# Kernel tuning notes

Measured on AMD Instinct MI355X. Metric: run time of the kernel, lower is better.

Reference implementation:

```python
import jax, jax.numpy as jnp
import numpy as np
from jax.scipy.special import logsumexp

VOCAB = 32000
NUM_STATE = 512
BATCH = 64
MAXLEN = 256


def setup_inputs() -> dict:
    key = jax.random.key(0)
    k1, k2, k3, k4 = jax.random.split(key, 4)
    sentences = jax.random.randint(k1, (BATCH, MAXLEN), 0, VOCAB, dtype=jnp.int64 if jax.config.jax_enable_x64 else jnp.int32)
    masks = jnp.ones((BATCH, MAXLEN), dtype=jnp.float32)
    # parameters: uniform(-0.5, 0.5) as in reset_parameter
    input_w = jax.random.uniform(k2, (VOCAB, NUM_STATE), jnp.float32, -0.5, 0.5)
    transition = jax.random.uniform(k3, (NUM_STATE, NUM_STATE), jnp.float32, -0.5, 0.5)
    begin = jax.random.uniform(k4, (NUM_STATE,), jnp.float32, -0.5, 0.5)
    return {"sentences": sentences, "masks": masks, "input_w": input_w,
            "transition": transition, "begin": begin}


def reference(sentences, masks, input_w, transition, begin):
    batch, maxlen = sentences.shape
    S = begin.shape[0]
    # emission log-probs: log_softmax over dim 0 (vocab axis) — as in original
    norm_input = jax.nn.log_softmax(input_w, axis=0)            # [V, S]
    emis = norm_input[sentences.T]                               # [maxlen, batch, S]
    T = jax.nn.log_softmax(transition, axis=-1)                  # [S, S]

    def bmv(bv):
        # logsumexp(T[None] + bv[:, None, :], axis=-1) -> [batch, S]
        return logsumexp(T[None, :, :] + bv[:, None, :], axis=-1)

    fwd0 = jnp.broadcast_to(jax.nn.log_softmax(begin, axis=0), (batch, S))
    m0 = bmv(fwd0)                                               # [batch, S]
    # NOTE: original normalizes over dim=0 (the BATCH axis) via logsoftmax0
    m1 = bmv(jax.nn.log_softmax(m0 + emis[0], axis=0))

    # Original loop bug replicated: pre_forward = mid_forwards[i-1], so the
    # recurrence is lagged: m_{i+1} = f(m_{i-1}, e_i) for i >= 1.
    def step(carry, e):
        a, b = carry                                             # a = m_{i-1}, b = m_i
        m = bmv(jax.nn.log_softmax(a + e, axis=0))               # m_{i+1}
        return (b, m), m

    (_, _), ms = jax.lax.scan(step, (m0, m1), emis[1:maxlen - 1])
    hidden = jnp.concatenate([m0[None], m1[None], ms], axis=0)   # [maxlen, batch, S]

    pred_prob = hidden + emis
    ppl = logsumexp(pred_prob, axis=-1) * masks.T                # [maxlen, batch]
    return jnp.sum(ppl)
```

## Files before the change

kernel.cpp:

```cpp
#include <hip/hip_runtime.h>
#include <math.h>

#define VV 32000
#define SS 512
#define BB 64
#define TT 256
#define NS 128
#define NPART 500
#define NCB 128
#define WSLOT (BB * SS)


__global__ void k_zero(float* __restrict__ out, float* __restrict__ colsum,
                       unsigned* __restrict__ flags) {
  const int t = threadIdx.x;
  if (t == 0) out[0] = 0.f;
  if (t < 256) flags[t] = 0u;
  colsum[t] = 0.f;
}

__global__ void k_colpart(const float* __restrict__ iw, float* __restrict__ psum) {
  const int blk = blockIdx.x;
  const int tid = threadIdx.x;
  const int cg = tid & 127;
  const int rh = tid >> 7;
  const int r0 = blk * 128 + rh * 64;
  const float4* iw4 = (const float4*)iw;
  float4 s = make_float4(0.f, 0.f, 0.f, 0.f);
  #pragma unroll 4
  for (int r = 0; r < 64; ++r) {
    float4 x = iw4[(size_t)(r0 + r) * 128 + cg];
    s.x += __expf(x.x); s.y += __expf(x.y); s.z += __expf(x.z); s.w += __expf(x.w);
  }
  ((float4*)psum)[(size_t)(blk * 2 + rh) * 128 + cg] = s;
}

__global__ void k_colreduce(const float* __restrict__ psum, float* __restrict__ colsum) {
  const int c = threadIdx.x;
  const int p0 = blockIdx.x * 20;
  float s = 0.f;
  #pragma unroll 5
  for (int p = 0; p < 20; ++p) s += psum[(size_t)(p0 + p) * SS + c];
  atomicAdd(&colsum[c], s);
}

__global__ void k_lse(const float* __restrict__ colsum, float* __restrict__ colLSE) {
  colLSE[threadIdx.x] = __logf(colsum[threadIdx.x]);
}

__global__ void k_begin(const float* __restrict__ begin, float* __restrict__ sb) {
  __shared__ float red[8];
  const int tid = threadIdx.x;
  float x = begin[tid];
  float m = x;
  #pragma unroll
  for (int o = 32; o; o >>= 1) m = fmaxf(m, __shfl_xor(m, o));
  if ((tid & 63) == 0) red[tid >> 6] = m;
  __syncthreads();
  float bm = red[0];
  for (int i = 1; i < 8; ++i) bm = fmaxf(bm, red[i]);
  __syncthreads();
  float e = __expf(x - bm);
  float s = e;
  #pragma unroll
  for (int o = 32; o; o >>= 1) s += __shfl_xor(s, o);
  if ((tid & 63) == 0) red[tid >> 6] = s;
  __syncthreads();
  float tot = 0.f;
  for (int i = 0; i < 8; ++i) tot += red[i];
  sb[tid] = e / tot;
}

__global__ void k_transP(const float* __restrict__ trans, const float* __restrict__ sb,
                         float* __restrict__ P, float* __restrict__ q0vec) {
  const int i = blockIdx.x;
  const int lane = threadIdx.x;
  const float* rp = trans + (size_t)i * SS;
  float xs[8];
  float m = -1e30f;
  #pragma unroll
  for (int cc = 0; cc < 8; ++cc) { xs[cc] = rp[cc * 64 + lane]; m = fmaxf(m, xs[cc]); }
  #pragma unroll
  for (int o = 32; o; o >>= 1) m = fmaxf(m, __shfl_xor(m, o));
  float s = 0.f;
  #pragma unroll
  for (int cc = 0; cc < 8; ++cc) s += __expf(xs[cc] - m);
  #pragma unroll
  for (int o = 32; o; o >>= 1) s += __shfl_xor(s, o);
  const float lse = m + __logf(s);
  float qa = 0.f;
  #pragma unroll
  for (int cc = 0; cc < 8; ++cc) {
    float p = __expf(xs[cc] - lse);
    P[(size_t)i * SS + cc * 64 + lane] = p;
    qa += p * sb[cc * 64 + lane];
  }
  #pragma unroll
  for (int o = 32; o; o >>= 1) qa += __shfl_xor(qa, o);
  if (lane == 0) q0vec[i] = qa;
}

__global__ __launch_bounds__(256) void k_persist(
    const float* __restrict__ P, const float* __restrict__ q0vec,
    const float* __restrict__ iw, const float* __restrict__ colLSE,
    const int* __restrict__ sent, float* __restrict__ wring,
    float* __restrict__ dotpart, unsigned* __restrict__ flags) {
  const int c = blockIdx.x & 1;
  const int g = blockIdx.x >> 1;
  const int lane = threadIdx.x & 63;
  const int h = __builtin_amdgcn_readfirstlane(threadIdx.x >> 6);
  const int i0 = g << 2;
  const int kmax = c ? 127 : 128;
  unsigned* const myflags = flags + (c << 7);

  const float4 cl = *(const float4*)(colLSE + i0);
  const float4* const P0 = (const float4*)(P + (size_t)(i0 + 0) * SS) + h * 32;
  const float4* const P1 = (const float4*)(P + (size_t)(i0 + 1) * SS) + h * 32;
  const float4* const P2 = (const float4*)(P + (size_t)(i0 + 2) * SS) + h * 32;
  const float4* const P3 = (const float4*)(P + (size_t)(i0 + 3) * SS) + h * 32;

  __shared__ float4 red[4][64];

  for (int k = 0; k <= kmax; ++k) {
    const int t0 = 2 * k;
    const int tw = t0 + c;
    const int td = tw - 1;
    const bool doW = (h == 0) && (tw <= 254);
    const bool doD = (h == 1) && (td >= 0);

    float4 ivW = make_float4(0.f, 0.f, 0.f, 0.f);
    float4 ivD = make_float4(0.f, 0.f, 0.f, 0.f);
    if (doW) {
      const int row = sent[lane * TT + tw];
      ivW = *(const float4*)(iw + (size_t)row * SS + i0);
    }
    if (doD) {
      const int row = sent[lane * TT + td];
      ivD = *(const float4*)(iw + (size_t)row * SS + i0);
    }

    if (k > 0) {
      __syncthreads();
      if (h == 0) {
        const unsigned tgt = (unsigned)k;
        for (;;) {
          const unsigned va = __hip_atomic_load(myflags + lane, __ATOMIC_RELAXED,
                                                __HIP_MEMORY_SCOPE_AGENT);
          const unsigned vb = __hip_atomic_load(myflags + 64 + lane, __ATOMIC_RELAXED,
                                                __HIP_MEMORY_SCOPE_AGENT);
          if (__all((va >= tgt) && (vb >= tgt))) break;
          __builtin_amdgcn_s_sleep(2);
        }
      }
      __syncthreads();
    }

    float a0 = 0.f, a1 = 0.f, a2 = 0.f, a3 = 0.f;
    if (t0 == 0) {
      if (h == 0) {
        a0 = q0vec[i0 + 0]; a1 = q0vec[i0 + 1];
        a2 = q0vec[i0 + 2]; a3 = q0vec[i0 + 3];
      }
    } else {
      const float4* wv = (const float4*)(wring + (size_t)(tw - 2) * WSLOT)
                         + (size_t)h * 32 * 64;
      float4 wr[32];
      #pragma unroll
      for (int u = 0; u < 32; ++u) wr[u] = wv[u * 64 + lane];
      #pragma unroll
      for (int u = 0; u < 32; ++u) {
        const float4 p0 = P0[u];
        const float4 p1 = P1[u];
        const float4 p2 = P2[u];
        const float4 p3 = P3[u];
        a0 += wr[u].x * p0.x + wr[u].y * p0.y + wr[u].z * p0.z + wr[u].w * p0.w;
        a1 += wr[u].x * p1.x + wr[u].y * p1.y + wr[u].z * p1.z + wr[u].w * p1.w;
        a2 += wr[u].x * p2.x + wr[u].y * p2.y + wr[u].z * p2.z + wr[u].w * p2.w;
        a3 += wr[u].x * p3.x + wr[u].y * p3.y + wr[u].z * p3.z + wr[u].w * p3.w;
      }
    }

    red[h][lane] = make_float4(a0, a1, a2, a3);
    __syncthreads();

    if (h < 2) {
      const float4 r0 = red[0][lane], r1 = red[1][lane];
      const float4 r2 = red[2][lane], r3 = red[3][lane];
      const float s0 = (r0.x + r1.x) + (r2.x + r3.x);
      const float s1 = (r0.y + r1.y) + (r2.y + r3.y);
      const float s2 = (r0.z + r1.z) + (r2.z + r3.z);
      const float s3 = (r0.w + r1.w) + (r2.w + r3.w);

      if (doW) {
        float w0 = s0 * __expf(ivW.x - cl.x);
        float w1 = s1 * __expf(ivW.y - cl.y);
        float w2 = s2 * __expf(ivW.z - cl.z);
        float w3 = s3 * __expf(ivW.w - cl.w);
        float c0 = w0, c1 = w1, c2 = w2, c3 = w3;
        #pragma unroll
        for (int o = 32; o; o >>= 1) {
          c0 += __shfl_xor(c0, o);
          c1 += __shfl_xor(c1, o);
          c2 += __shfl_xor(c2, o);
          c3 += __shfl_xor(c3, o);
        }
        union { float2 f; unsigned long long u; } lo, hi;
        lo.f = make_float2(w0 / c0, w1 / c1);
        hi.f = make_float2(w2 / c2, w3 / c3);
        unsigned long long* wd = (unsigned long long*)
            ((float4*)(wring + (size_t)tw * WSLOT) + (g * 64 + lane));
        __hip_atomic_store(wd, lo.u, __ATOMIC_RELAXED, __HIP_MEMORY_SCOPE_AGENT);
        __hip_atomic_store(wd + 1, hi.u, __ATOMIC_RELAXED, __HIP_MEMORY_SCOPE_AGENT);
        asm volatile("s_waitcnt vmcnt(0)" ::: "memory");
        if (lane == 0)
          __hip_atomic_store(&myflags[g], (unsigned)(k + 1), __ATOMIC_RELAXED,
                             __HIP_MEMORY_SCOPE_AGENT);
      }

      if (doD) {
        const float dp = s0 * __expf(ivD.x - cl.x)
                       + s1 * __expf(ivD.y - cl.y)
                       + s2 * __expf(ivD.z - cl.z)
                       + s3 * __expf(ivD.w - cl.w);
        dotpart[((size_t)td * NS + g) * BB + lane] = dp;
      }
    }
  }
}

__global__ void k_final(const float* __restrict__ dotpart, const float* __restrict__ masks,
                        float* __restrict__ out) {
  const int t = blockIdx.x;
  const int tid = threadIdx.x;
  const int b = tid & 63, g = tid >> 6;
  float sum = 0.f;
  for (int s = g; s < NS; s += 4) sum += dotpart[((size_t)t * NS + s) * BB + b];
  __shared__ float red[4][64];
  red[g][b] = sum;
  __syncthreads();
  if (g == 0) {
    float tot = (red[0][b] + red[1][b]) + (red[2][b] + red[3][b]);
    float v = __logf(tot) * masks[b * TT + t];
    #pragma unroll
    for (int o = 32; o; o >>= 1) v += __shfl_xor(v, o);
    if (b == 0) atomicAdd(out, v);
  }
}

extern "C" void kernel_launch(void* const* d_in, const int* in_sizes, int n_in,
                              void* d_out, int out_size, void* d_ws, size_t ws_size,
                              hipStream_t stream) {
  const int* sent = (const int*)d_in[0];
  const float* masks = (const float*)d_in[1];
  const float* iw = (const float*)d_in[2];
  const float* trans = (const float*)d_in[3];
  const float* begin = (const float*)d_in[4];
  float* out = (float*)d_out;
  float* ws = (float*)d_ws;

  float* P = ws;
  float* colLSE = P + 262144;
  float* psum = colLSE + 512;
  float* colsum = psum + 256000;
  float* sb = colsum + 512;
  float* q0vec = sb + 512;
  float* dotpart = q0vec + 512;
  unsigned* flags = (unsigned*)(dotpart + 2097152);
  float* wring = (float*)flags + 512;

  k_zero<<<1, 512, 0, stream>>>(out, colsum, flags);
  k_colpart<<<250, 256, 0, stream>>>(iw, psum);
  k_colreduce<<<25, 512, 0, stream>>>(psum, colsum);
  k_lse<<<1, 512, 0, stream>>>(colsum, colLSE);
  k_begin<<<1, 512, 0, stream>>>(begin, sb);
  k_transP<<<512, 64, 0, stream>>>(trans, sb, P, q0vec);

  {
    const float* Pp = P;
    const float* q0p = q0vec;
    const float* iwp = iw;
    const float* clp = colLSE;
    const int* sentp = sent;
    float* wrp = wring;
    float* dpp = dotpart;
    unsigned* fp = flags;
    void* args[] = {&Pp, &q0p, &iwp, &clp, &sentp, &wrp, &dpp, &fp};
    (void)hipLaunchCooperativeKernel((const void*)k_persist, dim3(256), dim3(256),
                                     args, 0, stream);
  }

  k_final<<<TT, 256, 0, stream>>>(dotpart, masks, out);
}
```

Baseline: 786.9 us.

## Fold small prep kernels and split per-step flag sync across waves

Removes the zero, log-sum-exp and begin-softmax kernels by folding their work into k_colpart, k_transP and the persistent kernel, which cuts launch overhead. Inside the persistent recurrence, each wave now polls the flags itself instead of relying on two block barriers around a single polling wave. The normalized-weight write is split across two waves with separate low and high flag arrays, and the reduction buffer is double-buffered so one barrier per step is enough. This shortens the per-step critical path of the serial chain, at the cost of more spin traffic on the flags from every wave.

```diff
diff --git a/kernel.cpp b/kernel.cpp
--- a/kernel.cpp
+++ b/kernel.cpp
@@ -6,22 +6,19 @@
 #define BB 64
 #define TT 256
 #define NS 128
-#define NPART 500
-#define NCB 128
 #define WSLOT (BB * SS)
 
 
-__global__ void k_zero(float* __restrict__ out, float* __restrict__ colsum,
-                       unsigned* __restrict__ flags) {
-  const int t = threadIdx.x;
-  if (t == 0) out[0] = 0.f;
-  if (t < 256) flags[t] = 0u;
-  colsum[t] = 0.f;
-}
-
-__global__ void k_colpart(const float* __restrict__ iw, float* __restrict__ psum) {
+__global__ void k_colpart(const float* __restrict__ iw, float* __restrict__ psum,
+                          float* __restrict__ out, float* __restrict__ colsum,
+                          unsigned* __restrict__ flags) {
   const int blk = blockIdx.x;
   const int tid = threadIdx.x;
+  if (blk == 0) {
+    if (tid == 0) out[0] = 0.f;
+    flags[tid] = 0u; flags[tid + 256] = 0u;
+    colsum[tid] = 0.f; colsum[tid + 256] = 0.f;
+  }
   const int cg = tid & 127;
   const int rh = tid >> 7;
   const int r0 = blk * 128 + rh * 64;
@@ -44,37 +41,23 @@
   atomicAdd(&colsum[c], s);
 }
 
-__global__ void k_lse(const float* __restrict__ colsum, float* __restrict__ colLSE) {
-  colLSE[threadIdx.x] = __logf(colsum[threadIdx.x]);
-}
-
-__global__ void k_begin(const float* __restrict__ begin, float* __restrict__ sb) {
-  __shared__ float red[8];
-  const int tid = threadIdx.x;
-  float x = begin[tid];
-  float m = x;
-  #pragma unroll
-  for (int o = 32; o; o >>= 1) m = fmaxf(m, __shfl_xor(m, o));
-  if ((tid & 63) == 0) red[tid >> 6] = m;
-  __syncthreads();
-  float bm = red[0];
-  for (int i = 1; i < 8; ++i) bm = fmaxf(bm, red[i]);
-  __syncthreads();
-  float e = __expf(x - bm);
-  float s = e;
-  #pragma unroll
-  for (int o = 32; o; o >>= 1) s += __shfl_xor(s, o);
-  if ((tid & 63) == 0) red[tid >> 6] = s;
-  __syncthreads();
-  float tot = 0.f;
-  for (int i = 0; i < 8; ++i) tot += red[i];
-  sb[tid] = e / tot;
-}
-
-__global__ void k_transP(const float* __restrict__ trans, const float* __restrict__ sb,
+__global__ void k_transP(const float* __restrict__ trans, const float* __restrict__ begin,
                          float* __restrict__ P, float* __restrict__ q0vec) {
   const int i = blockIdx.x;
   const int lane = threadIdx.x;
+  float bx[8];
+  float bm = -1e30f;
+  #pragma unroll
+  for (int cc = 0; cc < 8; ++cc) { bx[cc] = begin[cc * 64 + lane]; bm = fmaxf(bm, bx[cc]); }
+  #pragma unroll
+  for (int o = 32; o; o >>= 1) bm = fmaxf(bm, __shfl_xor(bm, o));
+  float bs = 0.f;
+  #pragma unroll
+  for (int cc = 0; cc < 8; ++cc) { bx[cc] = __expf(bx[cc] - bm); bs += bx[cc]; }
+  #pragma unroll
+  for (int o = 32; o; o >>= 1) bs += __shfl_xor(bs, o);
+  const float binv = 1.f / bs;
+
   const float* rp = trans + (size_t)i * SS;
   float xs[8];
   float m = -1e30f;
@@ -93,7 +76,7 @@
   for (int cc = 0; cc < 8; ++cc) {
     float p = __expf(xs[cc] - lse);
     P[(size_t)i * SS + cc * 64 + lane] = p;
-    qa += p * sb[cc * 64 + lane];
+    qa += p * (bx[cc] * binv);
   }
   #pragma unroll
   for (int o = 32; o; o >>= 1) qa += __shfl_xor(qa, o);
@@ -102,7 +85,7 @@
 
 __global__ __launch_bounds__(256) void k_persist(
     const float* __restrict__ P, const float* __restrict__ q0vec,
-    const float* __restrict__ iw, const float* __restrict__ colLSE,
+    const float* __restrict__ iw, const float* __restrict__ colsum,
     const int* __restrict__ sent, float* __restrict__ wring,
     float* __restrict__ dotpart, unsigned* __restrict__ flags) {
   const int c = blockIdx.x & 1;
@@ -111,22 +94,28 @@
   const int h = __builtin_amdgcn_readfirstlane(threadIdx.x >> 6);
   const int i0 = g << 2;
   const int kmax = c ? 127 : 128;
-  unsigned* const myflags = flags + (c << 7);
-
-  const float4 cl = *(const float4*)(colLSE + i0);
+  unsigned* const flagL = flags + (c << 7);
+  unsigned* const flagH = flags + 256 + (c << 7);
+  const int gp = (h << 5) + (lane & 31);
+
+  float4 cl;
+  cl.x = __logf(colsum[i0 + 0]); cl.y = __logf(colsum[i0 + 1]);
+  cl.z = __logf(colsum[i0 + 2]); cl.w = __logf(colsum[i0 + 3]);
+
   const float4* const P0 = (const float4*)(P + (size_t)(i0 + 0) * SS) + h * 32;
   const float4* const P1 = (const float4*)(P + (size_t)(i0 + 1) * SS) + h * 32;
   const float4* const P2 = (const float4*)(P + (size_t)(i0 + 2) * SS) + h * 32;
   const float4* const P3 = (const float4*)(P + (size_t)(i0 + 3) * SS) + h * 32;
 
-  __shared__ float4 red[4][64];
+  __shared__ float4 red[2][4][64];
 
   for (int k = 0; k <= kmax; ++k) {
+    const int rb = k & 1;
     const int t0 = 2 * k;
     const int tw = t0 + c;
     const int td = tw - 1;
-    const bool doW = (h == 0) && (tw <= 254);
-    const bool doD = (h == 1) && (td >= 0);
+    const bool doW = (h <= 1) && (tw <= 254);
+    const bool doD = (h == 2) && (td >= 0);
 
     float4 ivW = make_float4(0.f, 0.f, 0.f, 0.f);
     float4 ivD = make_float4(0.f, 0.f, 0.f, 0.f);
@@ -140,19 +129,15 @@
     }
 
     if (k > 0) {
-      __syncthreads();
-      if (h == 0) {
-        const unsigned tgt = (unsigned)k;
-        for (;;) {
-          const unsigned va = __hip_atomic_load(myflags + lane, __ATOMIC_RELAXED,
-                                                __HIP_MEMORY_SCOPE_AGENT);
-          const unsigned vb = __hip_atomic_load(myflags + 64 + lane, __ATOMIC_RELAXED,
-                                                __HIP_MEMORY_SCOPE_AGENT);
-          if (__all((va >= tgt) && (vb >= tgt))) break;
-          __builtin_amdgcn_s_sleep(2);
-        }
-      }
-      __syncthreads();
+      const unsigned tgt = (unsigned)k;
+      for (;;) {
+        const unsigned va = __hip_atomic_load(flagL + gp, __ATOMIC_RELAXED,
+                                              __HIP_MEMORY_SCOPE_AGENT);
+        const unsigned vb = __hip_atomic_load(flagH + gp, __ATOMIC_RELAXED,
+                                              __HIP_MEMORY_SCOPE_AGENT);
+        if (__all((va >= tgt) && (vb >= tgt))) break;
+      }
+      asm volatile("" ::: "memory");
     }
 
     float a0 = 0.f, a1 = 0.f, a2 = 0.f, a3 = 0.f;
@@ -180,50 +165,57 @@
       }
     }
 
-    red[h][lane] = make_float4(a0, a1, a2, a3);
+    red[rb][h][lane] = make_float4(a0, a1, a2, a3);
     __syncthreads();
 
-    if (h < 2) {
-      const float4 r0 = red[0][lane], r1 = red[1][lane];
-      const float4 r2 = red[2][lane], r3 = red[3][lane];
+    if (doW) {
+      const float4 r0 = red[rb][0][lane], r1 = red[rb][1][lane];
+      const float4 r2 = red[rb][2][lane], r3 = red[rb][3][lane];
+      unsigned long long* wd = (unsigned long long*)
+          ((float4*)(wring + (size_t)tw * WSLOT) + (g * 64 + lane));
+      if (h == 0) {
+        const float s0 = (r0.x + r1.x) + (r2.x + r3.x);
+        const float s1 = (r0.y + r1.y) + (r2.y + r3.y);
+        float w0 = s0 * __expf(ivW.x - cl.x);
+        float w1 = s1 * __expf(ivW.y - cl.y);
+        float c0 = w0, c1 = w1;
+        #pragma unroll
+        for (int o = 32; o; o >>= 1) { c0 += __shfl_xor(c0, o); c1 += __shfl_xor(c1, o); }
+        union { float2 f; unsigned long long u; } lo;
+        lo.f = make_float2(w0 / c0, w1 / c1);
+        __hip_atomic_store(wd, lo.u, __ATOMIC_RELAXED, __HIP_MEMORY_SCOPE_AGENT);
+        asm volatile("s_waitcnt vmcnt(0)" ::: "memory");
+        if (lane == 0)
+          __hip_atomic_store(&flagL[g], (unsigned)(k + 1), __ATOMIC_RELAXED,
+                             __HIP_MEMORY_SCOPE_AGENT);
+      } else {
+        const float s2 = (r0.z + r1.z) + (r2.z + r3.z);
+        const float s3 = (r0.w + r1.w) + (r2.w + r3.w);
+        float w2 = s2 * __expf(ivW.z - cl.z);
+        float w3 = s3 * __expf(ivW.w - cl.w);
+        float c2 = w2, c3 = w3;
+        #pragma unroll
+        for (int o = 32; o; o >>= 1) { c2 += __shfl_xor(c2, o); c3 += __shfl_xor(c3, o); }
+        union { float2 f; unsigned long long u; } hi;
+        hi.f = make_float2(w2 / c2, w3 / c3);
+        __hip_atomic_store(wd + 1, hi.u, __ATOMIC_RELAXED, __HIP_MEMORY_SCOPE_AGENT);
+        asm volatile("s_waitcnt vmcnt(0)" ::: "memory");
+        if (lane == 0)
+          __hip_atomic_store(&flagH[g], (unsigned)(k + 1), __ATOMIC_RELAXED,
+                             __HIP_MEMORY_SCOPE_AGENT);
+      }
+    } else if (doD) {
+      const float4 r0 = red[rb][0][lane], r1 = red[rb][1][lane];
+      const float4 r2 = red[rb][2][lane], r3 = red[rb][3][lane];
       const float s0 = (r0.x + r1.x) + (r2.x + r3.x);
       const float s1 = (r0.y + r1.y) + (r2.y + r3.y);
       const float s2 = (r0.z + r1.z) + (r2.z + r3.z);
       const float s3 = (r0.w + r1.w) + (r2.w + r3.w);
-
-      if (doW) {
-        float w0 = s0 * __expf(ivW.x - cl.x);
-        float w1 = s1 * __expf(ivW.y - cl.y);
-        float w2 = s2 * __expf(ivW.z - cl.z);
-        float w3 = s3 * __expf(ivW.w - cl.w);
-        float c0 = w0, c1 = w1, c2 = w2, c3 = w3;
-        #pragma unroll
-        for (int o = 32; o; o >>= 1) {
-          c0 += __shfl_xor(c0, o);
-          c1 += __shfl_xor(c1, o);
-          c2 += __shfl_xor(c2, o);
-          c3 += __shfl_xor(c3, o);
-        }
-        union { float2 f; unsigned long long u; } lo, hi;
-        lo.f = make_float2(w0 / c0, w1 / c1);
-        hi.f = make_float2(w2 / c2, w3 / c3);
-        unsigned long long* wd = (unsigned long long*)
-            ((float4*)(wring + (size_t)tw * WSLOT) + (g * 64 + lane));
-        __hip_atomic_store(wd, lo.u, __ATOMIC_RELAXED, __HIP_MEMORY_SCOPE_AGENT);
-        __hip_atomic_store(wd + 1, hi.u, __ATOMIC_RELAXED, __HIP_MEMORY_SCOPE_AGENT);
-        asm volatile("s_waitcnt vmcnt(0)" ::: "memory");
-        if (lane == 0)
-          __hip_atomic_store(&myflags[g], (unsigned)(k + 1), __ATOMIC_RELAXED,
-                             __HIP_MEMORY_SCOPE_AGENT);
-      }
-
-      if (doD) {
-        const float dp = s0 * __expf(ivD.x - cl.x)
-                       + s1 * __expf(ivD.y - cl.y)
-                       + s2 * __expf(ivD.z - cl.z)
-                       + s3 * __expf(ivD.w - cl.w);
-        dotpart[((size_t)td * NS + g) * BB + lane] = dp;
-      }
+      const float dp = s0 * __expf(ivD.x - cl.x)
+                     + s1 * __expf(ivD.y - cl.y)
+                     + s2 * __expf(ivD.z - cl.z)
+                     + s3 * __expf(ivD.w - cl.w);
+      dotpart[((size_t)td * NS + g) * BB + lane] = dp;
     }
   }
 }
@@ -259,32 +251,27 @@
   float* ws = (float*)d_ws;
 
   float* P = ws;
-  float* colLSE = P + 262144;
-  float* psum = colLSE + 512;
+  float* psum = P + 262144;
   float* colsum = psum + 256000;
-  float* sb = colsum + 512;
-  float* q0vec = sb + 512;
+  float* q0vec = colsum + 512;
   float* dotpart = q0vec + 512;
   unsigned* flags = (unsigned*)(dotpart + 2097152);
   float* wring = (float*)flags + 512;
 
-  k_zero<<<1, 512, 0, stream>>>(out, colsum, flags);
-  k_colpart<<<250, 256, 0, stream>>>(iw, psum);
+  k_colpart<<<250, 256, 0, stream>>>(iw, psum, out, colsum, flags);
   k_colreduce<<<25, 512, 0, stream>>>(psum, colsum);
-  k_lse<<<1, 512, 0, stream>>>(colsum, colLSE);
-  k_begin<<<1, 512, 0, stream>>>(begin, sb);
-  k_transP<<<512, 64, 0, stream>>>(trans, sb, P, q0vec);
+  k_transP<<<512, 64, 0, stream>>>(trans, begin, P, q0vec);
 
   {
     const float* Pp = P;
     const float* q0p = q0vec;
     const float* iwp = iw;
-    const float* clp = colLSE;
+    const float* csp = colsum;
     const int* sentp = sent;
     float* wrp = wring;
     float* dpp = dotpart;
     unsigned* fp = flags;
-    void* args[] = {&Pp, &q0p, &iwp, &clp, &sentp, &wrp, &dpp, &fp};
+    void* args[] = {&Pp, &q0p, &iwp, &csp, &sentp, &wrp, &dpp, &fp};
     (void)hipLaunchCooperativeKernel((const void*)k_persist, dim3(256), dim3(256),
                                      args, 0, stream);
   }
```

Result: slower. 1.136 ms (+44.4%).
